# Optimization experiments

Hardware: AMD Instinct MI355X
Metric: run time of the kernel (lower is better)

The kernel has to match this reference:

```python
import jax, jax.numpy as jnp
import numpy as np

B, L, E, H, NL = 2, 1024, 1024, 16, 3
D = E // H
SCALE = D ** -0.5
EPS = 1e-5


def rmsnorm(x, g):
    return x * jax.lax.rsqrt(jnp.mean(x * x, axis=-1, keepdims=True) + EPS) * g


def rope(x, cos, sin):
    # x: (B, m*L, H, D); cos/sin: (L, D). Tile cos/sin to the growing KV length
    # (the source broadcasts rel_pos over the concatenated cache).
    m = x.shape[1] // cos.shape[0]
    c = jnp.tile(cos, (m, 1))[None, :, None, :]
    s = jnp.tile(sin, (m, 1))[None, :, None, :]
    x1, x2 = jnp.split(x, 2, axis=-1)
    rot = jnp.concatenate([-x2, x1], axis=-1)  # rotate_half convention
    return x * c + rot * s


def setup_inputs() -> dict:
    key = jax.random.key(0)
    ks = jax.random.split(key, 8)
    x = jax.random.normal(ks[0], (B, L, E), jnp.float32)
    inv_freq = 1.0 / (10000.0 ** (jnp.arange(0, D, 2, dtype=jnp.float32) / D))
    t = jnp.arange(L, dtype=jnp.float32)[:, None] * inv_freq[None, :]  # (L, D/2)
    cos = jnp.concatenate([jnp.cos(t), jnp.cos(t)], axis=-1)
    sin = jnp.concatenate([jnp.sin(t), jnp.sin(t)], axis=-1)
    attn_mask = jnp.where(jnp.tril(jnp.ones((L, L), bool)), 0.0, -jnp.inf).astype(jnp.float32)
    w_scale = E ** -0.5  # ~kaiming_uniform fan_in magnitude
    Wq = jax.random.normal(ks[1], (NL, E, E), jnp.float32) * w_scale
    Wk = jax.random.normal(ks[2], (NL, E, E), jnp.float32) * w_scale
    Wv = jax.random.normal(ks[3], (NL, E, E), jnp.float32) * w_scale
    Wo = jax.random.normal(ks[4], (E, E), jnp.float32) * w_scale
    lambdas = jax.random.normal(ks[5], (NL,), jnp.float32)
    g_ln = jnp.ones((NL, E), jnp.float32)
    g_final = jnp.ones((E,), jnp.float32)
    alpha = jnp.ones((1,), jnp.float32)
    return dict(x=x, cos=cos, sin=sin, attn_mask=attn_mask, Wq=Wq, Wk=Wk, Wv=Wv,
                g_ln=g_ln, lambdas=lambdas, Wo=Wo, g_final=g_final, alpha=alpha)


def reference(x, cos, sin, attn_mask, Wq, Wk, Wv, g_ln, lambdas, Wo, g_final, alpha):
    # lambda weights: sigmoid then non-affine LayerNorm across the NL layers
    s = jax.nn.sigmoid(lambdas)
    lw = (s - s.mean()) * jax.lax.rsqrt(s.var() + EPS)

    acc_k, acc_v = [], []
    outs = []
    for i in range(NL):
        q = (x @ Wq[i].T).reshape(B, L, H, D)
        k = (x @ Wk[i].T).reshape(B, L, H, D)
        v = (x @ Wv[i].T).reshape(B, L, H, D)
        if i > 0:  # prepend-current growing KV cache (source concatenates [k, accumulated])
            k = jnp.concatenate([k] + acc_k, axis=1)
            v = jnp.concatenate([v] + acc_v, axis=1)
        q = rope(q, cos, sin)
        k = rope(k, cos, sin)
        KV = k.shape[1]
        scores = jnp.einsum('bqhd,bkhd->bhqk', q * SCALE, k)  # (B,H,L,KV)
        if i == 0:
            m = attn_mask
        else:  # source fills everything past tgt_len with -inf
            m = jnp.concatenate(
                [attn_mask, jnp.full((L, KV - L), -jnp.inf, attn_mask.dtype)], axis=1)
        w = jax.nn.softmax(scores + m, axis=-1)
        a = jnp.einsum('bhqk,bkhd->bqhd', w, v).reshape(B, L, E)
        outs.append(rmsnorm(a, g_ln[i]) * lw[i])
        acc_k.append(k)  # stores the full concatenated, roped k (lengths 1L,2L,4L)
        acc_v.append(v)
    combined = outs[0] + outs[1] + outs[2]
    out = rmsnorm(combined + alpha * x, g_final)
    return out @ Wo.T
```

## Files before the change

### kernel.cpp

```cpp
#include <hip/hip_runtime.h>


#define B_  2
#define L_  1024
#define E_  1024
#define H_  16
#define NL_ 3
#define D_  64

typedef __bf16 bf16_t;
typedef __bf16 bf16x8 __attribute__((ext_vector_type(8)));
typedef __bf16 bf16x4 __attribute__((ext_vector_type(4)));
typedef float  f32x4  __attribute__((ext_vector_type(4)));

#define NEG_INF (-__builtin_inff())

typedef const __attribute__((address_space(1))) void* gas_ptr;
typedef __attribute__((address_space(3))) void* las_ptr;

#define GLD_LDS16(gp, lp) \
  __builtin_amdgcn_global_load_lds((gas_ptr)(gp), (las_ptr)(lp), 16, 0, 0)

__global__ __launch_bounds__(256) void cvt_k(
    const float* __restrict__ s0, const float* __restrict__ s1,
    const float* __restrict__ s2, const float* __restrict__ s3,
    const float* __restrict__ s4, bf16_t* __restrict__ d0,
    bf16_t* __restrict__ d1, bf16_t* __restrict__ d2, bf16_t* __restrict__ d3,
    bf16_t* __restrict__ d4)
{
  const int seg = blockIdx.y;
  const float* s;
  bf16_t* d;
  int n;
  if (seg == 0)      { s = s0; d = d0; n = 3145728; }
  else if (seg == 1) { s = s1; d = d1; n = 3145728; }
  else if (seg == 2) { s = s2; d = d2; n = 3145728; }
  else if (seg == 3) { s = s3; d = d3; n = 1048576; }
  else               { s = s4; d = d4; n = 2097152; }
  const int i = (blockIdx.x * 256 + threadIdx.x) * 4;
  if (i < n) {
    const float4 v = *(const float4*)(s + i);
    bf16x4 o;
    o[0] = (bf16_t)v.x; o[1] = (bf16_t)v.y; o[2] = (bf16_t)v.z; o[3] = (bf16_t)v.w;
    *(bf16x4*)(d + i) = o;
  }
}

template <int EPI>
__global__ __launch_bounds__(256) void gemm_k(
    const bf16_t* __restrict__ X, const bf16_t* __restrict__ W0,
    const bf16_t* __restrict__ W1, const bf16_t* __restrict__ W2,
    const float* __restrict__ cosb, const float* __restrict__ sinb,
    bf16_t* __restrict__ qk, bf16_t* __restrict__ vt, float* __restrict__ outf)
{
  __shared__ bf16_t smem[128 * 128];
  const int tid = threadIdx.x;
  const int lane = tid & 63;
  const int w = tid >> 6;
  const int q4 = lane >> 4, l15 = lane & 15;
  const int row0swz = (l15 >> 1) & 3;

  const int flat0 = blockIdx.y * 16 + blockIdx.x;
  const int chunk = (EPI ? 128 : 1152) >> 3;
  const int nf = (flat0 & 7) * chunk + (flat0 >> 3);
  const int bxs = nf & 15;
  const int bys = nf >> 4;

  const int row0 = bxs * 128;

  int g, tileN;
  const bf16_t* Wb;
  if (EPI == 0) {
    g = bys >> 3;
    tileN = bys & 7;
    const int t = g % 3, il = g / 3;
    Wb = (t == 0 ? W0 : (t == 1 ? W1 : W2)) + (size_t)il * E_ * E_;
  } else {
    g = 0;
    tileN = bys;
    Wb = W0;
  }
  const int col0 = tileN * 128;
  const int rA = (w & 1) * 64;
  const int cB = (w >> 1) * 64;

  const int srow = tid >> 2;
  const int sgcol = (((tid & 3) ^ ((tid >> 3) & 3)) << 3);

  f32x4 acc[4][4] = {};

  const size_t xrow = (size_t)(row0 + srow) * E_ + sgcol;
  const size_t xrow2 = xrow + (size_t)64 * E_;
  const size_t wrow = (size_t)(col0 + srow) * E_ + sgcol;
  const size_t wrow2 = wrow + (size_t)64 * E_;

#define STAGE_(buf, k0_)                                         \
  do {                                                           \
    bf16_t* Xb = smem + (buf) * 8192;                            \
    bf16_t* Wbl = smem + (buf) * 8192 + 4096;                    \
    GLD_LDS16(X + xrow + (k0_), &Xb[tid * 8]);                   \
    GLD_LDS16(X + xrow2 + (k0_), &Xb[2048 + tid * 8]);           \
    GLD_LDS16(Wb + wrow + (k0_), &Wbl[tid * 8]);                 \
    GLD_LDS16(Wb + wrow2 + (k0_), &Wbl[2048 + tid * 8]);         \
  } while (0)

#define COMPUTE_(buf)                                            \
  do {                                                           \
    const bf16_t* Xb = smem + (buf) * 8192;                      \
    const bf16_t* Wbl = smem + (buf) * 8192 + 4096;              \
    bf16x8 a[4], b[4];                                           \
    const int slot = (q4 ^ row0swz) << 3;                        \
    _Pragma("unroll")                                            \
    for (int mi = 0; mi < 4; ++mi)                               \
      a[mi] = *(const bf16x8*)&Xb[(rA + mi * 16 + l15) * 32 + slot]; \
    _Pragma("unroll")                                            \
    for (int ni = 0; ni < 4; ++ni)                               \
      b[ni] = *(const bf16x8*)&Wbl[(cB + ni * 16 + l15) * 32 + slot]; \
    _Pragma("unroll")                                            \
    for (int mi = 0; mi < 4; ++mi)                               \
      _Pragma("unroll")                                          \
      for (int ni = 0; ni < 4; ++ni)                             \
        acc[mi][ni] = __builtin_amdgcn_mfma_f32_16x16x32_bf16(   \
            a[mi], b[ni], acc[mi][ni], 0, 0, 0);                 \
  } while (0)

  STAGE_(0, 0);
  __syncthreads();
  int cur = 0;
  for (int k0 = 32; k0 < E_; k0 += 32) {
    STAGE_(cur ^ 1, k0);
    COMPUTE_(cur);
    __syncthreads();
    cur ^= 1;
  }
  COMPUTE_(cur);

#undef STAGE_
#undef COMPUTE_

  if (EPI == 0) {
    const int t = g % 3, il = g / 3;
    if (t < 2) {
      const int slot = il * 2 + t;
      const int h = tileN * 2 + (w >> 1);
      const float post = (t == 0) ? 0.18033688011112042f : 1.0f;
#pragma unroll
      for (int mi = 0; mi < 4; ++mi) {
#pragma unroll
        for (int reg = 0; reg < 4; ++reg) {
          const int m = row0 + rA + mi * 16 + q4 * 4 + reg;
          const int b = m >> 10, l = m & (L_ - 1);
#pragma unroll
          for (int ni = 0; ni < 4; ++ni) {
            const int d = ni * 16 + l15;
            const float v0 = acc[mi][ni][reg];
            const float part = acc[mi][ni ^ 2][reg];
            const float rot = (d < 32) ? -part : part;
            const float v = (v0 * cosb[l * D_ + d] + rot * sinb[l * D_ + d]) * post;
            qk[(((size_t)slot * B_ + b) * H_ + h) * ((size_t)L_ * D_) +
               (size_t)l * D_ + d] = (bf16_t)v;
          }
        }
      }
    } else {
      const int n_l = tid >> 1, lh = tid & 1;
      const int h = tileN * 2 + (n_l >> 6), d = n_l & 63;
      const int bb = row0 >> 10;
      __syncthreads();
#pragma unroll
      for (int p = 0; p < 2; ++p) {
        if ((w & 1) == p) {
#pragma unroll
          for (int mi = 0; mi < 4; ++mi)
#pragma unroll
            for (int reg = 0; reg < 4; ++reg)
#pragma unroll
              for (int ni = 0; ni < 4; ++ni)
                smem[(cB + ni * 16 + l15) * 72 + mi * 16 + q4 * 4 + reg] =
                    (bf16_t)acc[mi][ni][reg];
        }
        __syncthreads();
        const int l0 = (row0 & (L_ - 1)) + p * 64 + lh * 32;
        bf16_t* gp = vt + (((size_t)il * B_ + bb) * H_ + h) * ((size_t)D_ * L_) +
                     (size_t)d * L_ + l0;
        const bf16_t* sp = &smem[n_l * 72 + lh * 32];
#pragma unroll
        for (int c = 0; c < 4; ++c)
          *(bf16x8*)(gp + c * 8) = *(const bf16x8*)(sp + c * 8);
        if (p == 0) __syncthreads();
      }
    }
  } else {
#pragma unroll
    for (int mi = 0; mi < 4; ++mi) {
#pragma unroll
      for (int reg = 0; reg < 4; ++reg) {
        const int m = row0 + rA + mi * 16 + q4 * 4 + reg;
#pragma unroll
        for (int ni = 0; ni < 4; ++ni) {
          const int n = col0 + cB + ni * 16 + l15;
          outf[(size_t)m * E_ + n] = acc[mi][ni][reg];
        }
      }
    }
  }
}

__global__ __launch_bounds__(256) void attn_k(const bf16_t* __restrict__ qk,
                                              const bf16_t* __restrict__ vt,
                                              bf16_t* __restrict__ attn)
{
  __shared__ bf16_t Ks[2][64 * 64];
  __shared__ bf16_t Vts[2][64 * 64];
  __shared__ bf16_t Ps[4][16 * 72];

  const int tid = threadIdx.x, lane = tid & 63, w = tid >> 6;
  const int q4 = lane >> 4, l15 = lane & 15;

  const int flat0 = blockIdx.y * 8 + blockIdx.x;
  const int nf = (flat0 & 7) * 96 + (flat0 >> 3);
  const int x = nf & 7;
  const int by = nf >> 3;

  const int h = by & 15, b = (by >> 4) & 1, i = by >> 5;
  const size_t HD = (size_t)L_ * D_;
  const bf16_t* Qp = qk + (((size_t)(i * 2 + 0) * B_ + b) * H_ + h) * HD;
  const bf16_t* Kp = qk + (((size_t)(i * 2 + 1) * B_ + b) * H_ + h) * HD;
  const bf16_t* Vp = vt + (((size_t)i * B_ + b) * H_ + h) * HD;

  const int srow = tid >> 3;
  const int sg = tid & 7;
  const int scol = (sg ^ (srow & 7)) * 8;

  bf16x8 ones;
#pragma unroll
  for (int jj = 0; jj < 8; ++jj) ones[jj] = (bf16_t)1.0f;

#pragma unroll 1
  for (int ph = 0; ph < 2; ++ph) {
    const int qt = ph == 0 ? (15 - x) : x;

    bf16x8 aq[2];
#pragma unroll
    for (int kk = 0; kk < 2; ++kk)
      aq[kk] = *(const bf16x8*)(Qp + (size_t)(qt * 64 + w * 16 + l15) * 64 +
                                kk * 32 + q4 * 8);

    if (ph == 1) __syncthreads();
#pragma unroll
    for (int it = 0; it < 2; ++it) {
      const int flat = it * 2048 + tid * 8;
      const int r = it * 32 + srow;
      GLD_LDS16(Kp + r * 64 + scol, &Ks[0][flat]);
      GLD_LDS16(Vp + (size_t)r * L_ + scol, &Vts[0][flat]);
    }

    f32x4 o[4] = {};
    f32x4 lacc = {};

#pragma unroll 1
    for (int j = 0; j <= qt; ++j) {
      __syncthreads();
      const int cur = j & 1;
      if (j < qt) {
        const int nxt = cur ^ 1;
#pragma unroll
        for (int it = 0; it < 2; ++it) {
          const int flat = it * 2048 + tid * 8;
          const int r = it * 32 + srow;
          GLD_LDS16(Kp + (j + 1) * 4096 + r * 64 + scol, &Ks[nxt][flat]);
          GLD_LDS16(Vp + (size_t)r * L_ + (j + 1) * 64 + scol, &Vts[nxt][flat]);
        }
      }

      f32x4 s[4] = {};
#pragma unroll
      for (int kk = 0; kk < 2; ++kk) {
#pragma unroll
        for (int ni = 0; ni < 4; ++ni) {
          const bf16x8 bk =
              *(const bf16x8*)&Ks[cur][(ni * 16 + l15) * 64 +
                                       (((kk * 4 + q4) ^ (l15 & 7)) << 3)];
          s[ni] = __builtin_amdgcn_mfma_f32_16x16x32_bf16(aq[kk], bk, s[ni], 0, 0, 0);
        }
      }

      if (j == qt) {
#pragma unroll
        for (int reg = 0; reg < 4; ++reg)
#pragma unroll
          for (int ni = 0; ni < 4; ++ni)
            if (ni * 16 + l15 > w * 16 + q4 * 4 + reg) s[ni][reg] = NEG_INF;
      }

#pragma unroll
      for (int reg = 0; reg < 4; ++reg)
#pragma unroll
        for (int ni = 0; ni < 4; ++ni)
          Ps[w][(q4 * 4 + reg) * 72 + ni * 16 + l15] = (bf16_t)exp2f(s[ni][reg]);
      asm volatile("s_waitcnt lgkmcnt(0)" ::: "memory");

#pragma unroll
      for (int kk = 0; kk < 2; ++kk) {
        const bf16x8 ap = *(const bf16x8*)&Ps[w][l15 * 72 + kk * 32 + q4 * 8];
        lacc = __builtin_amdgcn_mfma_f32_16x16x32_bf16(ap, ones, lacc, 0, 0, 0);
#pragma unroll
        for (int di = 0; di < 4; ++di) {
          const bf16x8 bv =
              *(const bf16x8*)&Vts[cur][(di * 16 + l15) * 64 +
                                        (((kk * 4 + q4) ^ (l15 & 7)) << 3)];
          o[di] = __builtin_amdgcn_mfma_f32_16x16x32_bf16(ap, bv, o[di], 0, 0, 0);
        }
      }
    }

    const int row_base = (i * B_ + b) * L_ + qt * 64 + w * 16 + q4 * 4;
#pragma unroll
    for (int reg = 0; reg < 4; ++reg) {
      const float inv = 1.f / lacc[reg];
      const int r = row_base + reg;
#pragma unroll
      for (int di = 0; di < 4; ++di)
        attn[(size_t)r * E_ + h * 64 + di * 16 + l15] = (bf16_t)(o[di][reg] * inv);
    }
  }
}

__device__ __forceinline__ float block_sum(float v, float* sm)
{
#pragma unroll
  for (int off = 32; off > 0; off >>= 1) v += __shfl_xor(v, off);
  const int w = threadIdx.x >> 6;
  __syncthreads();
  if ((threadIdx.x & 63) == 0) sm[w] = v;
  __syncthreads();
  return sm[0] + sm[1] + sm[2] + sm[3];
}

__global__ __launch_bounds__(256) void combine_k(
    const bf16_t* __restrict__ attn, const float* __restrict__ x,
    const float* __restrict__ g_ln, const float* __restrict__ lambdas,
    const float* __restrict__ g_final, const float* __restrict__ alphap,
    bf16_t* __restrict__ xn)
{
  __shared__ float sm[4];
  const int row = blockIdx.x;
  const int tid = threadIdx.x;

  float sg[3], lw[3];
#pragma unroll
  for (int i = 0; i < 3; ++i) sg[i] = 1.f / (1.f + expf(-lambdas[i]));
  const float mean = (sg[0] + sg[1] + sg[2]) * (1.f / 3.f);
  const float var = ((sg[0] - mean) * (sg[0] - mean) + (sg[1] - mean) * (sg[1] - mean) +
                     (sg[2] - mean) * (sg[2] - mean)) * (1.f / 3.f);
  const float rv = rsqrtf(var + 1e-5f);
#pragma unroll
  for (int i = 0; i < 3; ++i) lw[i] = (sg[i] - mean) * rv;

  const float av = alphap[0];
  float c[4];
#pragma unroll
  for (int k = 0; k < 4; ++k) {
    const int e = tid + k * 256;
    c[k] = av * x[(size_t)row * E_ + e];
  }

  for (int i = 0; i < 3; ++i) {
    float a[4];
    float ss = 0.f;
#pragma unroll
    for (int k = 0; k < 4; ++k) {
      const int e = tid + k * 256;
      a[k] = (float)attn[((size_t)i * (B_ * L_) + row) * E_ + e];
      ss += a[k] * a[k];
    }
    ss = block_sum(ss, sm);
    const float rinv = rsqrtf(ss * (1.f / (float)E_) + 1e-5f);
#pragma unroll
    for (int k = 0; k < 4; ++k) {
      const int e = tid + k * 256;
      c[k] += a[k] * rinv * g_ln[i * E_ + e] * lw[i];
    }
  }

  float ss = 0.f;
#pragma unroll
  for (int k = 0; k < 4; ++k) ss += c[k] * c[k];
  ss = block_sum(ss, sm);
  const float rinv = rsqrtf(ss * (1.f / (float)E_) + 1e-5f);
#pragma unroll
  for (int k = 0; k < 4; ++k) {
    const int e = tid + k * 256;
    xn[(size_t)row * E_ + e] = (bf16_t)(c[k] * rinv * g_final[e]);
  }
}

extern "C" void kernel_launch(void* const* d_in, const int* in_sizes, int n_in,
                              void* d_out, int out_size, void* d_ws, size_t ws_size,
                              hipStream_t stream)
{
  const float* x       = (const float*)d_in[0];
  const float* cosb    = (const float*)d_in[1];
  const float* sinb    = (const float*)d_in[2];
  const float* Wq      = (const float*)d_in[4];
  const float* Wk      = (const float*)d_in[5];
  const float* Wv      = (const float*)d_in[6];
  const float* g_ln    = (const float*)d_in[7];
  const float* lambdas = (const float*)d_in[8];
  const float* Wo      = (const float*)d_in[9];
  const float* g_final = (const float*)d_in[10];
  const float* alphap  = (const float*)d_in[11];

  bf16_t* qk    = (bf16_t*)d_ws;
  bf16_t* VT    = (bf16_t*)((char*)d_ws + 25165824);
  bf16_t* attnb = (bf16_t*)((char*)d_ws + 37748736);
  bf16_t* Wqb   = (bf16_t*)((char*)d_ws + 50331648);
  bf16_t* Wkb   = Wqb + 3145728;
  bf16_t* Wvb   = Wkb + 3145728;
  bf16_t* Wob   = (bf16_t*)((char*)d_ws + 69206016);
  bf16_t* xb    = (bf16_t*)((char*)d_ws + 71303168);
  bf16_t* xnb   = (bf16_t*)d_ws;
  float*  out   = (float*)d_out;

  cvt_k<<<dim3(3072, 5), 256, 0, stream>>>(Wq, Wk, Wv, Wo, x, Wqb, Wkb, Wvb, Wob, xb);
  gemm_k<0><<<dim3(16, 72), 256, 0, stream>>>(xb, Wqb, Wkb, Wvb, cosb, sinb,
                                              qk, VT, nullptr);
  attn_k<<<dim3(8, 96), 256, 0, stream>>>(qk, VT, attnb);
  combine_k<<<dim3(B_ * L_), 256, 0, stream>>>(attnb, x, g_ln, lambdas, g_final,
                                               alphap, xnb);
  gemm_k<1><<<dim3(16, 8), 256, 0, stream>>>(xnb, Wob, Wob, Wob, cosb, sinb,
                                             nullptr, nullptr, out);
}
```

Measured before the change: 235.3 us.

## Fuse Q/K/V projections into one GEMM block sharing the X tile

Each block of the QKV projection kernel now computes the Q, K and V outputs for the same 128x128 tile, loading the X tile once and reusing it against three weight tiles. This cuts redundant X loads and shrinks the grid from 1152 to 384 blocks. The cost is 48 accumulator tiles per thread (192 f32 registers), which can reduce occupancy or spill, plus a larger 64KB LDS footprint. There are also fewer blocks to spread across the CUs. The output GEMM is split into its own non-templated kernel with unchanged logic.

```diff
diff --git a/kernel.cpp b/kernel.cpp
--- a/kernel.cpp
+++ b/kernel.cpp
@@ -46,14 +46,13 @@
   }
 }
 
-template <int EPI>
-__global__ __launch_bounds__(256) void gemm_k(
+__global__ __launch_bounds__(256) void gemmqkv_k(
     const bf16_t* __restrict__ X, const bf16_t* __restrict__ W0,
     const bf16_t* __restrict__ W1, const bf16_t* __restrict__ W2,
     const float* __restrict__ cosb, const float* __restrict__ sinb,
-    bf16_t* __restrict__ qk, bf16_t* __restrict__ vt, float* __restrict__ outf)
-{
-  __shared__ bf16_t smem[128 * 128];
+    bf16_t* __restrict__ qk, bf16_t* __restrict__ vt)
+{
+  __shared__ bf16_t smem[32768];
   const int tid = threadIdx.x;
   const int lane = tid & 63;
   const int w = tid >> 6;
@@ -61,26 +60,154 @@
   const int row0swz = (l15 >> 1) & 3;
 
   const int flat0 = blockIdx.y * 16 + blockIdx.x;
-  const int chunk = (EPI ? 128 : 1152) >> 3;
-  const int nf = (flat0 & 7) * chunk + (flat0 >> 3);
+  const int nf = (flat0 & 7) * 48 + (flat0 >> 3);
   const int bxs = nf & 15;
   const int bys = nf >> 4;
-
   const int row0 = bxs * 128;
-
-  int g, tileN;
-  const bf16_t* Wb;
-  if (EPI == 0) {
-    g = bys >> 3;
-    tileN = bys & 7;
-    const int t = g % 3, il = g / 3;
-    Wb = (t == 0 ? W0 : (t == 1 ? W1 : W2)) + (size_t)il * E_ * E_;
-  } else {
-    g = 0;
-    tileN = bys;
-    Wb = W0;
-  }
-  const int col0 = tileN * 128;
+  const int il = bys >> 3;
+  const int colTile = bys & 7;
+  const int col0 = colTile * 128;
+
+  const bf16_t* Wq = W0 + (size_t)il * E_ * E_;
+  const bf16_t* Wk = W1 + (size_t)il * E_ * E_;
+  const bf16_t* Wv = W2 + (size_t)il * E_ * E_;
+
+  const int rA = (w & 1) * 64;
+  const int cB = (w >> 1) * 64;
+
+  const int srow = tid >> 2;
+  const int sgcol = (((tid & 3) ^ ((tid >> 3) & 3)) << 3);
+
+  f32x4 acc[3][4][4] = {};
+
+  const size_t xrow = (size_t)(row0 + srow) * E_ + sgcol;
+  const size_t xrow2 = xrow + (size_t)64 * E_;
+  const size_t wrow = (size_t)(col0 + srow) * E_ + sgcol;
+  const size_t wrow2 = wrow + (size_t)64 * E_;
+
+#define STAGE_(buf, k0_)                                          \
+  do {                                                            \
+    bf16_t* bp = smem + (buf) * 16384;                            \
+    GLD_LDS16(X + xrow + (k0_), &bp[tid * 8]);                    \
+    GLD_LDS16(X + xrow2 + (k0_), &bp[2048 + tid * 8]);            \
+    GLD_LDS16(Wq + wrow + (k0_), &bp[4096 + tid * 8]);            \
+    GLD_LDS16(Wq + wrow2 + (k0_), &bp[6144 + tid * 8]);           \
+    GLD_LDS16(Wk + wrow + (k0_), &bp[8192 + tid * 8]);            \
+    GLD_LDS16(Wk + wrow2 + (k0_), &bp[10240 + tid * 8]);          \
+    GLD_LDS16(Wv + wrow + (k0_), &bp[12288 + tid * 8]);           \
+    GLD_LDS16(Wv + wrow2 + (k0_), &bp[14336 + tid * 8]);          \
+  } while (0)
+
+#define COMPUTE_(buf)                                             \
+  do {                                                            \
+    const bf16_t* bp = smem + (buf) * 16384;                      \
+    const int slot = (q4 ^ row0swz) << 3;                         \
+    bf16x8 a[4];                                                  \
+    _Pragma("unroll")                                             \
+    for (int mi = 0; mi < 4; ++mi)                                \
+      a[mi] = *(const bf16x8*)&bp[(rA + mi * 16 + l15) * 32 + slot]; \
+    _Pragma("unroll")                                             \
+    for (int m = 0; m < 3; ++m) {                                 \
+      bf16x8 b[4];                                                \
+      _Pragma("unroll")                                           \
+      for (int ni = 0; ni < 4; ++ni)                              \
+        b[ni] = *(const bf16x8*)&bp[4096 + m * 4096 +             \
+                                    (cB + ni * 16 + l15) * 32 + slot]; \
+      _Pragma("unroll")                                           \
+      for (int mi = 0; mi < 4; ++mi)                              \
+        _Pragma("unroll")                                         \
+        for (int ni = 0; ni < 4; ++ni)                            \
+          acc[m][mi][ni] = __builtin_amdgcn_mfma_f32_16x16x32_bf16( \
+              a[mi], b[ni], acc[m][mi][ni], 0, 0, 0);             \
+    }                                                             \
+  } while (0)
+
+  STAGE_(0, 0);
+  __syncthreads();
+  int cur = 0;
+  for (int k0 = 32; k0 < E_; k0 += 32) {
+    STAGE_(cur ^ 1, k0);
+    COMPUTE_(cur);
+    __syncthreads();
+    cur ^= 1;
+  }
+  COMPUTE_(cur);
+
+#undef STAGE_
+#undef COMPUTE_
+
+  const int h = colTile * 2 + (w >> 1);
+#pragma unroll
+  for (int t = 0; t < 2; ++t) {
+    const int slot = il * 2 + t;
+    const float post = (t == 0) ? 0.18033688011112042f : 1.0f;
+#pragma unroll
+    for (int mi = 0; mi < 4; ++mi) {
+#pragma unroll
+      for (int reg = 0; reg < 4; ++reg) {
+        const int m = row0 + rA + mi * 16 + q4 * 4 + reg;
+        const int b = m >> 10, l = m & (L_ - 1);
+#pragma unroll
+        for (int ni = 0; ni < 4; ++ni) {
+          const int d = ni * 16 + l15;
+          const float v0 = acc[t][mi][ni][reg];
+          const float part = acc[t][mi][ni ^ 2][reg];
+          const float rot = (d < 32) ? -part : part;
+          const float v = (v0 * cosb[l * D_ + d] + rot * sinb[l * D_ + d]) * post;
+          qk[(((size_t)slot * B_ + b) * H_ + h) * ((size_t)L_ * D_) +
+             (size_t)l * D_ + d] = (bf16_t)v;
+        }
+      }
+    }
+  }
+
+  {
+    const int n_l = tid >> 1, lh = tid & 1;
+    const int hv = colTile * 2 + (n_l >> 6), d = n_l & 63;
+    const int bb = row0 >> 10;
+    __syncthreads();
+#pragma unroll
+    for (int p = 0; p < 2; ++p) {
+      if ((w & 1) == p) {
+#pragma unroll
+        for (int mi = 0; mi < 4; ++mi)
+#pragma unroll
+          for (int reg = 0; reg < 4; ++reg)
+#pragma unroll
+            for (int ni = 0; ni < 4; ++ni)
+              smem[(cB + ni * 16 + l15) * 72 + mi * 16 + q4 * 4 + reg] =
+                  (bf16_t)acc[2][mi][ni][reg];
+      }
+      __syncthreads();
+      const int l0 = (row0 & (L_ - 1)) + p * 64 + lh * 32;
+      bf16_t* gp = vt + (((size_t)il * B_ + bb) * H_ + hv) * ((size_t)D_ * L_) +
+                   (size_t)d * L_ + l0;
+      const bf16_t* sp = &smem[n_l * 72 + lh * 32];
+#pragma unroll
+      for (int c = 0; c < 4; ++c)
+        *(bf16x8*)(gp + c * 8) = *(const bf16x8*)(sp + c * 8);
+      if (p == 0) __syncthreads();
+    }
+  }
+}
+
+__global__ __launch_bounds__(256) void wo_k(
+    const bf16_t* __restrict__ X, const bf16_t* __restrict__ W,
+    float* __restrict__ outf)
+{
+  __shared__ bf16_t smem[16384];
+  const int tid = threadIdx.x;
+  const int lane = tid & 63;
+  const int w = tid >> 6;
+  const int q4 = lane >> 4, l15 = lane & 15;
+  const int row0swz = (l15 >> 1) & 3;
+
+  const int flat0 = blockIdx.y * 16 + blockIdx.x;
+  const int nf = (flat0 & 7) * 16 + (flat0 >> 3);
+  const int bxs = nf & 15;
+  const int bys = nf >> 4;
+  const int row0 = bxs * 128;
+  const int col0 = bys * 128;
   const int rA = (w & 1) * 64;
   const int cB = (w >> 1) * 64;
 
@@ -100,8 +227,8 @@
     bf16_t* Wbl = smem + (buf) * 8192 + 4096;                    \
     GLD_LDS16(X + xrow + (k0_), &Xb[tid * 8]);                   \
     GLD_LDS16(X + xrow2 + (k0_), &Xb[2048 + tid * 8]);           \
-    GLD_LDS16(Wb + wrow + (k0_), &Wbl[tid * 8]);                 \
-    GLD_LDS16(Wb + wrow2 + (k0_), &Wbl[2048 + tid * 8]);         \
+    GLD_LDS16(W + wrow + (k0_), &Wbl[tid * 8]);                  \
+    GLD_LDS16(W + wrow2 + (k0_), &Wbl[2048 + tid * 8]);          \
   } while (0)
 
 #define COMPUTE_(buf)                                            \
@@ -138,69 +265,15 @@
 #undef STAGE_
 #undef COMPUTE_
 
-  if (EPI == 0) {
-    const int t = g % 3, il = g / 3;
-    if (t < 2) {
-      const int slot = il * 2 + t;
-      const int h = tileN * 2 + (w >> 1);
-      const float post = (t == 0) ? 0.18033688011112042f : 1.0f;
-#pragma unroll
-      for (int mi = 0; mi < 4; ++mi) {
-#pragma unroll
-        for (int reg = 0; reg < 4; ++reg) {
-          const int m = row0 + rA + mi * 16 + q4 * 4 + reg;
-          const int b = m >> 10, l = m & (L_ - 1);
-#pragma unroll
-          for (int ni = 0; ni < 4; ++ni) {
-            const int d = ni * 16 + l15;
-            const float v0 = acc[mi][ni][reg];
-            const float part = acc[mi][ni ^ 2][reg];
-            const float rot = (d < 32) ? -part : part;
-            const float v = (v0 * cosb[l * D_ + d] + rot * sinb[l * D_ + d]) * post;
-            qk[(((size_t)slot * B_ + b) * H_ + h) * ((size_t)L_ * D_) +
-               (size_t)l * D_ + d] = (bf16_t)v;
-          }
-        }
-      }
-    } else {
-      const int n_l = tid >> 1, lh = tid & 1;
-      const int h = tileN * 2 + (n_l >> 6), d = n_l & 63;
-      const int bb = row0 >> 10;
-      __syncthreads();
-#pragma unroll
-      for (int p = 0; p < 2; ++p) {
-        if ((w & 1) == p) {
-#pragma unroll
-          for (int mi = 0; mi < 4; ++mi)
-#pragma unroll
-            for (int reg = 0; reg < 4; ++reg)
-#pragma unroll
-              for (int ni = 0; ni < 4; ++ni)
-                smem[(cB + ni * 16 + l15) * 72 + mi * 16 + q4 * 4 + reg] =
-                    (bf16_t)acc[mi][ni][reg];
-        }
-        __syncthreads();
-        const int l0 = (row0 & (L_ - 1)) + p * 64 + lh * 32;
-        bf16_t* gp = vt + (((size_t)il * B_ + bb) * H_ + h) * ((size_t)D_ * L_) +
-                     (size_t)d * L_ + l0;
-        const bf16_t* sp = &smem[n_l * 72 + lh * 32];
-#pragma unroll
-        for (int c = 0; c < 4; ++c)
-          *(bf16x8*)(gp + c * 8) = *(const bf16x8*)(sp + c * 8);
-        if (p == 0) __syncthreads();
-      }
-    }
-  } else {
-#pragma unroll
-    for (int mi = 0; mi < 4; ++mi) {
-#pragma unroll
-      for (int reg = 0; reg < 4; ++reg) {
-        const int m = row0 + rA + mi * 16 + q4 * 4 + reg;
-#pragma unroll
-        for (int ni = 0; ni < 4; ++ni) {
-          const int n = col0 + cB + ni * 16 + l15;
-          outf[(size_t)m * E_ + n] = acc[mi][ni][reg];
-        }
+#pragma unroll
+  for (int mi = 0; mi < 4; ++mi) {
+#pragma unroll
+    for (int reg = 0; reg < 4; ++reg) {
+      const int m = row0 + rA + mi * 16 + q4 * 4 + reg;
+#pragma unroll
+      for (int ni = 0; ni < 4; ++ni) {
+        const int n = col0 + cB + ni * 16 + l15;
+        outf[(size_t)m * E_ + n] = acc[mi][ni][reg];
       }
     }
   }
@@ -423,11 +496,10 @@
   float*  out   = (float*)d_out;
 
   cvt_k<<<dim3(3072, 5), 256, 0, stream>>>(Wq, Wk, Wv, Wo, x, Wqb, Wkb, Wvb, Wob, xb);
-  gemm_k<0><<<dim3(16, 72), 256, 0, stream>>>(xb, Wqb, Wkb, Wvb, cosb, sinb,
-                                              qk, VT, nullptr);
+  gemmqkv_k<<<dim3(16, 24), 256, 0, stream>>>(xb, Wqb, Wkb, Wvb, cosb, sinb,
+                                              qk, VT);
   attn_k<<<dim3(8, 96), 256, 0, stream>>>(qk, VT, attnb);
   combine_k<<<dim3(B_ * L_), 256, 0, stream>>>(attnb, x, g_ln, lambdas, g_final,
                                                alphap, xnb);
-  gemm_k<1><<<dim3(16, 8), 256, 0, stream>>>(xnb, Wob, Wob, Wob, cosb, sinb,
-                                             nullptr, nullptr, out);
-}
+  wo_k<<<dim3(16, 8), 256, 0, stream>>>(xnb, Wob, out);
+}
```

Result: slower. 248.7 us (+5.7%).
